# Optimization experiments

Measured on AMD Instinct MI355X. Metric: run time of the kernel, lower is better.

Reference implementation:

```python
import jax, jax.numpy as jnp
import numpy as np

B, S, D = 2, 2048, 1024
H = 16
HD = D // H  # 64
ROPE_BASE = 10000.0


def rotate_half(x):
    x1, x2 = jnp.split(x, 2, axis=-1)
    return jnp.concatenate((-x2, x1), axis=-1)


def rope_cos_sin(seq_len, dim, dtype):
    inv_freq = 1.0 / (ROPE_BASE ** (jnp.arange(0, dim, 2, dtype=jnp.float32) / dim))
    t = jnp.arange(seq_len, dtype=jnp.float32)
    freqs = jnp.einsum('i,j->ij', t, inv_freq)          # [S, dim/2]
    emb = jnp.concatenate((freqs, freqs), axis=-1)      # [S, dim]
    return jnp.cos(emb).astype(dtype), jnp.sin(emb).astype(dtype)


def setup_inputs() -> dict:
    key = jax.random.key(0)
    ks = jax.random.split(key, 5)
    std = 0.02
    return {
        'x': jax.random.normal(ks[0], (B, S, D), dtype=jnp.float32),
        'wq': jax.random.normal(ks[1], (D, D), dtype=jnp.float32) * std,
        'wk': jax.random.normal(ks[2], (D, D), dtype=jnp.float32) * std,
        'wv': jax.random.normal(ks[3], (D, D), dtype=jnp.float32) * std,
        'wo': jax.random.normal(ks[4], (D, D), dtype=jnp.float32) * std,
    }


def reference(x, wq, wk, wv, wo):
    b, s, d = x.shape
    # Q/K/V projections (nn.Linear: x @ W.T)
    q = jnp.einsum('bsd,ed->bse', x, wq).reshape(b, s, H, HD).transpose(0, 2, 1, 3)
    k = jnp.einsum('bsd,ed->bse', x, wk).reshape(b, s, H, HD).transpose(0, 2, 1, 3)
    v = jnp.einsum('bsd,ed->bse', x, wv).reshape(b, s, H, HD).transpose(0, 2, 1, 3)
    # RoPE
    cos, sin = rope_cos_sin(s, HD, x.dtype)  # [s, HD]
    cos = cos[None, None]  # [1,1,s,HD]
    sin = sin[None, None]
    q = q * cos + rotate_half(q) * sin
    k = k * cos + rotate_half(k) * sin
    # Causal SDPA
    scale = HD ** -0.5
    scores = jnp.einsum('bhqd,bhkd->bhqk', q, k) * scale
    causal = jnp.tril(jnp.ones((s, s), dtype=bool))
    scores = jnp.where(causal[None, None], scores, jnp.finfo(scores.dtype).min)
    attn = jax.nn.softmax(scores, axis=-1)
    out = jnp.einsum('bhqk,bhkd->bhqd', attn, v)
    out = out.transpose(0, 2, 1, 3).reshape(b, s, d)
    return jnp.einsum('bsd,ed->bse', out, wo)
```

## Files before the change

kernel.cpp:

```cpp
#include <hip/hip_runtime.h>
#include <hip/hip_bf16.h>
#include <cstdint>
#include <cstddef>

#define BDIM 2
#define SDIM 2048
#define DDIM 1024
#define HN   16
#define HDIM 64

using bf16 = __bf16;
typedef __attribute__((ext_vector_type(8))) __bf16 bf16x8;
typedef __attribute__((ext_vector_type(4))) __bf16 bf16x4;
typedef __attribute__((ext_vector_type(4))) float  f32x4;

#define MFMA16(a, b, c) __builtin_amdgcn_mfma_f32_16x16x32_bf16((a), (b), (c), 0, 0, 0)

#define ASYNC16(g, l)                                                          \
  __builtin_amdgcn_global_load_lds(                                            \
      (const __attribute__((address_space(1))) void*)(g),                      \
      (__attribute__((address_space(3))) void*)(l), 16, 0, 0)

#define QSCALE 0.1803368801111204f

struct Ptr5 { const float* p[5]; };
__global__ __launch_bounds__(256) void cvt_all(Ptr5 srcs, bf16* __restrict__ xb,
                                               bf16* __restrict__ wb) {
  const int NX4 = (BDIM * SDIM * DDIM) / 4;
  int i = blockIdx.x * 256 + threadIdx.x;
  const float* src;
  bf16* dst;
  int j;
  if (i < NX4) {
    src = srcs.p[0]; dst = xb; j = i;
  } else {
    int k = i - NX4;
    int seg = k >> 18;
    j = k & 262143;
    src = srcs.p[seg + 1];
    dst = wb + (size_t)seg * (DDIM * DDIM) / 1;
    dst += 0;
    j = j;
    dst = wb + (size_t)seg * (DDIM * DDIM);
  }
  float4 v = ((const float4*)src)[j];
  bf16x4 o = {(__bf16)v.x, (__bf16)v.y, (__bf16)v.z, (__bf16)v.w};
  *(bf16x4*)(dst + (size_t)j * 4) = o;
}

__global__ __launch_bounds__(256) void rope_table(float* __restrict__ cosT,
                                                  float* __restrict__ sinT) {
  int i = blockIdx.x * 256 + threadIdx.x;
  int s = i >> 5, j = i & 31;
  float inv = powf(10000.f, -(float)j * (1.f / 32.f));
  float a = (float)s * inv;
  float sn, c;
  sincosf(a, &sn, &c);
  cosT[s * 64 + j]      = c;
  cosT[s * 64 + j + 32] = c;
  sinT[s * 64 + j]      = sn;
  sinT[s * 64 + j + 32] = sn;
}

__global__ __launch_bounds__(256) void fixup_qk(bf16* __restrict__ q,
                                                bf16* __restrict__ k,
                                                const float* __restrict__ cosT,
                                                const float* __restrict__ sinT) {
  const int bh = blockIdx.y;
  const int s = blockIdx.x * 32 + (threadIdx.x >> 3);
  const int j0 = (threadIdx.x & 7) * 4;
  const size_t base = ((size_t)bh * SDIM + s) * HDIM;
  const float4 c4 = *(const float4*)(cosT + s * 64 + j0);
  const float4 s4 = *(const float4*)(sinT + s * 64 + j0);
  const float cc[4] = {c4.x, c4.y, c4.z, c4.w};
  const float ss[4] = {s4.x, s4.y, s4.z, s4.w};

  bf16x4 qlo = *(bf16x4*)(q + base + j0);
  bf16x4 qhi = *(bf16x4*)(q + base + j0 + 32);
  bf16x4 klo = *(bf16x4*)(k + base + j0);
  bf16x4 khi = *(bf16x4*)(k + base + j0 + 32);
  bf16x4 rql, rqh, rkl, rkh;
#pragma unroll
  for (int e = 0; e < 4; ++e) {
    float a = (float)qlo[e], b = (float)qhi[e];
    rql[e] = (__bf16)((a * cc[e] - b * ss[e]) * QSCALE);
    rqh[e] = (__bf16)((b * cc[e] + a * ss[e]) * QSCALE);
    a = (float)klo[e]; b = (float)khi[e];
    rkl[e] = (__bf16)(a * cc[e] - b * ss[e]);
    rkh[e] = (__bf16)(b * cc[e] + a * ss[e]);
  }
  *(bf16x4*)(q + base + j0)      = rql;
  *(bf16x4*)(q + base + j0 + 32) = rqh;
  *(bf16x4*)(k + base + j0)      = rkl;
  *(bf16x4*)(k + base + j0 + 32) = rkh;
}

__global__ __launch_bounds__(256) void gemm_qkv(const bf16* __restrict__ A,
                                                const bf16* __restrict__ B0,
                                                bf16* __restrict__ C0,
                                                bf16* __restrict__ Vt) {
  constexpr int K = 1024;
  __shared__ __align__(16) bf16 As[128 * 64];
  __shared__ __align__(16) bf16 Bs[128 * 64];
  const int tid = threadIdx.x;
  const int l = tid & 63, w = tid >> 6;
  const int wr = w >> 1, wc = w & 1;
  const int lr = l & 15, lg = l >> 4;
  const int bm = blockIdx.y * 128;
  const int bn = blockIdx.x * 128;
  const bf16* Bw = B0 + (size_t)blockIdx.z * (1024 * 1024);

  f32x4 acc[4][4] = {};

  for (int k0 = 0; k0 < K; k0 += 64) {
    __syncthreads();
#pragma unroll
    for (int i = 0; i < 4; ++i) {
      int idx = i * 2048 + tid * 8;
      int row = idx >> 6, col = idx & 63;
      ASYNC16(A + (size_t)(bm + row) * K + (k0 + col), As + idx);
      ASYNC16(Bw + (size_t)(bn + row) * K + (k0 + col), Bs + idx);
    }
    __syncthreads();
#pragma unroll
    for (int c = 0; c < 2; ++c) {
      bf16x8 af[4], bfr[4];
#pragma unroll
      for (int m = 0; m < 4; ++m)
        af[m] = *(const bf16x8*)(As + (wr * 64 + m * 16 + lr) * 64 + c * 32 + lg * 8);
#pragma unroll
      for (int n = 0; n < 4; ++n)
        bfr[n] = *(const bf16x8*)(Bs + (wc * 64 + n * 16 + lr) * 64 + c * 32 + lg * 8);
      __builtin_amdgcn_s_setprio(1);
#pragma unroll
      for (int m = 0; m < 4; ++m)
#pragma unroll
        for (int n = 0; n < 4; ++n)
          acc[m][n] = MFMA16(af[m], bfr[n], acc[m][n]);
      __builtin_amdgcn_s_setprio(0);
    }
  }

  const int z = blockIdx.z;
  if (z < 2) {
    bf16* C = C0 + (size_t)z * ((size_t)BDIM * SDIM * DDIM);
#pragma unroll
    for (int m = 0; m < 4; ++m)
#pragma unroll
      for (int n = 0; n < 4; ++n)
#pragma unroll
        for (int r = 0; r < 4; ++r) {
          int row = bm + wr * 64 + m * 16 + lg * 4 + r;
          int col = bn + wc * 64 + n * 16 + lr;
          size_t off = (((size_t)(row >> 11) * HN + (col >> 6)) * SDIM + (row & (SDIM - 1))) * HDIM + (col & 63);
          C[off] = (__bf16)acc[m][n][r];
        }
  } else {
#pragma unroll
    for (int m = 0; m < 4; ++m) {
      const int row0 = bm + wr * 64 + m * 16 + lg * 4;
      const int bb = row0 >> 11, s0 = row0 & (SDIM - 1);
#pragma unroll
      for (int n = 0; n < 4; ++n) {
        const int col = bn + wc * 64 + n * 16 + lr;
        const int h = col >> 6, hd = col & 63;
        bf16x4 pv = {(__bf16)acc[m][n][0], (__bf16)acc[m][n][1],
                     (__bf16)acc[m][n][2], (__bf16)acc[m][n][3]};
        *(bf16x4*)(Vt + ((size_t)(bb * HN + h) * HDIM + hd) * SDIM + s0) = pv;
      }
    }
  }
}

__global__ __launch_bounds__(512) void gemm_out(const bf16* __restrict__ A,
                                                const bf16* __restrict__ Bw,
                                                float* __restrict__ C) {
  constexpr int K = 1024;
  __shared__ __align__(16) bf16 As[128 * 64];
  __shared__ __align__(16) bf16 Bs[128 * 64];
  const int tid = threadIdx.x;
  const int l = tid & 63, w = tid >> 6;
  const int wr = w >> 1, wc = w & 1;
  const int lr = l & 15, lg = l >> 4;
  const int bm = blockIdx.y * 128;
  const int bn = blockIdx.x * 128;

  f32x4 acc[2][4] = {};

  for (int k0 = 0; k0 < K; k0 += 64) {
    __syncthreads();
#pragma unroll
    for (int i = 0; i < 2; ++i) {
      int idx = i * 4096 + tid * 8;
      int row = idx >> 6, col = idx & 63;
      ASYNC16(A + (size_t)(bm + row) * K + (k0 + col), As + idx);
      ASYNC16(Bw + (size_t)(bn + row) * K + (k0 + col), Bs + idx);
    }
    __syncthreads();
#pragma unroll
    for (int c = 0; c < 2; ++c) {
      bf16x8 af[2], bfr[4];
#pragma unroll
      for (int m = 0; m < 2; ++m)
        af[m] = *(const bf16x8*)(As + (wr * 32 + m * 16 + lr) * 64 + c * 32 + lg * 8);
#pragma unroll
      for (int n = 0; n < 4; ++n)
        bfr[n] = *(const bf16x8*)(Bs + (wc * 64 + n * 16 + lr) * 64 + c * 32 + lg * 8);
      __builtin_amdgcn_s_setprio(1);
#pragma unroll
      for (int m = 0; m < 2; ++m)
#pragma unroll
        for (int n = 0; n < 4; ++n)
          acc[m][n] = MFMA16(af[m], bfr[n], acc[m][n]);
      __builtin_amdgcn_s_setprio(0);
    }
  }

#pragma unroll
  for (int m = 0; m < 2; ++m)
#pragma unroll
    for (int n = 0; n < 4; ++n)
#pragma unroll
      for (int r = 0; r < 4; ++r) {
        int row = bm + wr * 32 + m * 16 + lg * 4 + r;
        int col = bn + wc * 64 + n * 16 + lr;
        C[(size_t)row * DDIM + col] = acc[m][n][r];
      }
}

__global__ __launch_bounds__(512) void attn_fwd(const bf16* __restrict__ qg,
                                                const bf16* __restrict__ kg,
                                                const bf16* __restrict__ vtg,
                                                bf16* __restrict__ og) {
  __shared__ __align__(16) bf16 Sl[2][3][4096];
  __shared__ __align__(16) bf16 Pl[8][1024];

  const int tid = threadIdx.x;
  const int l = tid & 63, w = tid >> 6;
  const int g = w >> 2, wg = w & 3;
  const int lr = l & 15, lg = l >> 4;
  const int bh = blockIdx.x;
  const int qt = 31 - blockIdx.y;
  const int q0 = qt * 64;
  const size_t hb = (size_t)bh * SDIM * HDIM;
  const bf16* Q  = qg + hb;
  const bf16* Kp = kg + hb;
  const bf16* Vp = vtg + hb;
  const int b = bh >> 4, h = bh & 15;
  bf16* Pw = &Pl[w][0];
  const int swz = lr & 7;

  const int mm0 = 2 * wg, mm1 = 2 * wg + 1;
  const int f0 = mm0 & 3, c0 = mm0 >> 2;
  const int f1 = mm1 & 3, c1 = mm1 >> 2;
  const int lo0 = mm0 * 512 + l * 8;
  const int lo1 = mm1 * 512 + l * 8;
  bf16* const SlG = &Sl[g][0][0];

  bf16x8 qf[2];
#pragma unroll
  for (int c = 0; c < 2; ++c)
    qf[c] = *(const bf16x8*)(Q + (size_t)(q0 + wg * 16 + lr) * HDIM + c * 32 + lg * 8);

  f32x4 o[4] = {};
  float m = -3e38f, lsum = 0.f;

  const int ng   = (qt >= g) ? ((qt - g) >> 1) + 1 : 0;
  const int smax = (qt >> 1) + 1;

  const bf16* kN0 = Kp + (size_t)(f0 * 16 + lr) * HDIM + c0 * 32 + lg * 8 + (size_t)g * 64 * HDIM;
  const bf16* kN1 = Kp + (size_t)(f1 * 16 + lr) * HDIM + c1 * 32 + lg * 8 + (size_t)g * 64 * HDIM;
  const bf16* vN0 = Vp + (size_t)(f0 * 16 + lr) * SDIM + c0 * 32 + lg * 8 + g * 64;
  const bf16* vN1 = Vp + (size_t)(f1 * 16 + lr) * SDIM + c1 * 32 + lg * 8 + g * 64;

  if (ng > 0) {
    ASYNC16(kN0, SlG + 0 * 4096 + lo0); kN0 += 128 * HDIM;
    ASYNC16(kN1, SlG + 0 * 4096 + lo1); kN1 += 128 * HDIM;
    ASYNC16(vN0, SlG + 1 * 4096 + lo0); vN0 += 128;
    ASYNC16(vN1, SlG + 1 * 4096 + lo1); vN1 += 128;
  }
  __syncthreads();

  int ks = 0, vs = 1;
  for (int s = 0; s < smax; ++s) {
    const int t = 2 * s + g;
    const bool act = (s < ng);
    const int kn = 3 - ks - vs;
    const bool hasNext = act && (s + 1 < ng);

    if (hasNext) {
      ASYNC16(kN0, SlG + kn * 4096 + lo0); kN0 += 128 * HDIM;
      ASYNC16(kN1, SlG + kn * 4096 + lo1); kN1 += 128 * HDIM;
    }

    const bool diag = (t == qt);
    const int fLim = diag ? wg : 3;

    f32x4 sc[4] = {};
    if (act) {
      __builtin_amdgcn_s_setprio(1);
#pragma unroll
      for (int c = 0; c < 2; ++c)
#pragma unroll
        for (int f = 0; f < 4; ++f)
          if (f <= fLim) {
            bf16x8 kfr = *(const bf16x8*)(SlG + ks * 4096 + (c * 4 + f) * 512 + l * 8);
            sc[f] = MFMA16(kfr, qf[c], sc[f]);
          }
      __builtin_amdgcn_s_setprio(0);
    }

    __builtin_amdgcn_s_barrier();
    __builtin_amdgcn_sched_barrier(0);

    if (hasNext) {
      ASYNC16(vN0, SlG + ks * 4096 + lo0); vN0 += 128;
      ASYNC16(vN1, SlG + ks * 4096 + lo1); vN1 += 128;
    }

    if (act) {
      if (diag) {
#pragma unroll
        for (int f = 0; f < 4; ++f)
#pragma unroll
          for (int r = 0; r < 4; ++r) {
            if (f > wg)
              sc[f][r] = -3e38f;
            else if (f == wg)
              sc[f][r] = (lg * 4 + r <= lr) ? sc[f][r] : -3e38f;
          }
      }

      float mxl = -3e38f;
#pragma unroll
      for (int f = 0; f < 4; ++f)
#pragma unroll
        for (int r = 0; r < 4; ++r) mxl = fmaxf(mxl, sc[f][r]);

      if (!__all(mxl - m <= 8.f)) {
        float mx = fmaxf(mxl, __shfl_xor(mxl, 16));
        mx = fmaxf(mx, __shfl_xor(mx, 32));
        float mnew = fmaxf(m, mx);
        float corr = exp2f(m - mnew);
        m = mnew;
        lsum *= corr;
        float cb[4];
#pragma unroll
        for (int r = 0; r < 4; ++r) cb[r] = __shfl(corr, lg * 4 + r);
#pragma unroll
        for (int n = 0; n < 4; ++n)
#pragma unroll
          for (int r = 0; r < 4; ++r) o[n][r] *= cb[r];
      }

      float rs = 0.f;
#pragma unroll
      for (int f = 0; f < 4; ++f) {
        float p0 = exp2f(sc[f][0] - m);
        float p1 = exp2f(sc[f][1] - m);
        float p2 = exp2f(sc[f][2] - m);
        float p3 = exp2f(sc[f][3] - m);
        rs += (p0 + p1) + (p2 + p3);
        bf16x4 pv = {(__bf16)p0, (__bf16)p1, (__bf16)p2, (__bf16)p3};
        const int ch = f * 2 + (lg >> 1);
        *(bf16x4*)(Pw + lr * 64 + ((ch ^ swz) << 3) + (lg & 1) * 4) = pv;
      }
      lsum += rs;

      const int cLim = diag ? (wg >> 1) : 1;
      __builtin_amdgcn_s_setprio(1);
#pragma unroll
      for (int c = 0; c < 2; ++c)
        if (c <= cLim) {
          bf16x8 pf = *(const bf16x8*)(Pw + lr * 64 + (((c * 4 + lg) ^ swz) << 3));
#pragma unroll
          for (int n = 0; n < 4; ++n) {
            bf16x8 vfr = *(const bf16x8*)(SlG + vs * 4096 + (c * 4 + n) * 512 + l * 8);
            o[n] = MFMA16(pf, vfr, o[n]);
          }
        }
      __builtin_amdgcn_s_setprio(0);
    }

    __syncthreads();
    vs = ks;
    ks = kn;
  }

  float* Osh = (float*)&Sl[0][0][0];
  float* Msh = Osh + 4096;
  float* Lsh = Msh + 256;

  if (g == 1) {
    Msh[wg * 64 + l] = m;
    Lsh[wg * 64 + l] = lsum;
#pragma unroll
    for (int n = 0; n < 4; ++n)
#pragma unroll
      for (int r = 0; r < 4; ++r)
        Osh[((wg * 4 + n) * 4 + r) * 64 + l] = o[n][r];
  }
  __syncthreads();

  if (g == 0) {
    float m1 = Msh[wg * 64 + l], l1 = Lsh[wg * 64 + l];
    float mt = fmaxf(m, m1);
    float a0 = exp2f(m - mt), a1 = exp2f(m1 - mt);
    float lt = lsum * a0 + l1 * a1;
    lt += __shfl_xor(lt, 16);
    lt += __shfl_xor(lt, 32);
    float a0b[4], a1b[4], ltb[4];
#pragma unroll
    for (int r = 0; r < 4; ++r) {
      a0b[r] = __shfl(a0, lg * 4 + r);
      a1b[r] = __shfl(a1, lg * 4 + r);
      ltb[r] = __shfl(lt, lg * 4 + r);
    }
#pragma unroll
    for (int r = 0; r < 4; ++r) {
      float rl = 1.f / ltb[r];
      int qr = q0 + 16 * wg + lg * 4 + r;
#pragma unroll
      for (int n = 0; n < 4; ++n) {
        float o1 = Osh[((wg * 4 + n) * 4 + r) * 64 + l];
        og[((size_t)(b * SDIM + qr)) * DDIM + h * HDIM + n * 16 + lr] =
            (__bf16)((o[n][r] * a0b[r] + o1 * a1b[r]) * rl);
      }
    }
  }
}

extern "C" void kernel_launch(void* const* d_in, const int* in_sizes, int n_in,
                              void* d_out, int out_size, void* d_ws, size_t ws_size,
                              hipStream_t stream) {
  const float* x  = (const float*)d_in[0];
  const float* wq = (const float*)d_in[1];
  const float* wk = (const float*)d_in[2];
  const float* wv = (const float*)d_in[3];
  const float* wo = (const float*)d_in[4];

  char* ws = (char*)d_ws;
  const size_t MB = 1024 * 1024;
  bf16* xb   = (bf16*)(ws + 0);
  bf16* wqb  = (bf16*)(ws + 8 * MB);
  bf16* wob  = (bf16*)(ws + 14 * MB);
  bf16* qb   = (bf16*)(ws + 16 * MB);
  bf16* kb   = (bf16*)(ws + 24 * MB);
  bf16* vtb  = (bf16*)(ws + 32 * MB);
  bf16* ob   = (bf16*)(ws + 40 * MB);
  float* cosT = (float*)(ws + 48 * MB);
  float* sinT = (float*)(ws + 49 * MB);

  const int NX = BDIM * SDIM * DDIM;
  const int NW = DDIM * DDIM;

  Ptr5 srcs{{x, wq, wk, wv, wo}};
  cvt_all<<<(NX / 4 + NW) / 256, 256, 0, stream>>>(srcs, xb, wqb);
  rope_table<<<(SDIM * 32) / 256, 256, 0, stream>>>(cosT, sinT);
  gemm_qkv<<<dim3(8, 32, 3), 256, 0, stream>>>(xb, wqb, qb, vtb);
  fixup_qk<<<dim3(SDIM / 32, 32), 256, 0, stream>>>(qb, kb, cosT, sinT);
  attn_fwd<<<dim3(32, 32), 512, 0, stream>>>(qb, kb, vtb, ob);
  gemm_out<<<dim3(8, 32), 512, 0, stream>>>(ob, wob, (float*)d_out);
}
```

Before: 131.5 us.

## Load V fragments directly to registers and stage QKV epilogue through LDS

In the attention kernel, V tiles are no longer staged through shared memory. Each wave loads its V fragments straight from global memory into registers, which removes one LDS buffer and the mid-iteration barrier. The QKV GEMM epilogue for Q and K now writes through a padded shared-memory tile so each thread issues 16-byte row stores instead of scattered 2-byte stores. Direct V loads add global-load latency to each iteration and duplicate V reads across waves in exchange for less LDS traffic and fewer barriers. A dead-code cleanup in the conversion kernel is included.

```diff
diff --git a/kernel.cpp b/kernel.cpp
--- a/kernel.cpp
+++ b/kernel.cpp
@@ -38,9 +38,6 @@
     int seg = k >> 18;
     j = k & 262143;
     src = srcs.p[seg + 1];
-    dst = wb + (size_t)seg * (DDIM * DDIM) / 1;
-    dst += 0;
-    j = j;
     dst = wb + (size_t)seg * (DDIM * DDIM);
   }
   float4 v = ((const float4*)src)[j];
@@ -100,8 +97,9 @@
                                                 bf16* __restrict__ C0,
                                                 bf16* __restrict__ Vt) {
   constexpr int K = 1024;
-  __shared__ __align__(16) bf16 As[128 * 64];
-  __shared__ __align__(16) bf16 Bs[128 * 64];
+  __shared__ __align__(16) bf16 Sh[128 * 136];
+  bf16* const As = Sh;
+  bf16* const Bs = Sh + 8192;
   const int tid = threadIdx.x;
   const int l = tid & 63, w = tid >> 6;
   const int wr = w >> 1, wc = w & 1;
@@ -143,18 +141,25 @@
 
   const int z = blockIdx.z;
   if (z < 2) {
-    bf16* C = C0 + (size_t)z * ((size_t)BDIM * SDIM * DDIM);
+    __syncthreads();
 #pragma unroll
     for (int m = 0; m < 4; ++m)
 #pragma unroll
       for (int n = 0; n < 4; ++n)
 #pragma unroll
-        for (int r = 0; r < 4; ++r) {
-          int row = bm + wr * 64 + m * 16 + lg * 4 + r;
-          int col = bn + wc * 64 + n * 16 + lr;
-          size_t off = (((size_t)(row >> 11) * HN + (col >> 6)) * SDIM + (row & (SDIM - 1))) * HDIM + (col & 63);
-          C[off] = (__bf16)acc[m][n][r];
-        }
+        for (int r = 0; r < 4; ++r)
+          Sh[(wr * 64 + m * 16 + lg * 4 + r) * 136 + wc * 64 + n * 16 + lr] =
+              (__bf16)acc[m][n][r];
+    __syncthreads();
+    const int row_l = tid >> 1, cb = (tid & 1) * 64;
+    const int row = bm + row_l;
+    const int bb = row >> 11, s = row & (SDIM - 1);
+    const int h = (bn >> 6) + (tid & 1);
+    bf16* Cb = C0 + (size_t)z * ((size_t)BDIM * SDIM * DDIM) +
+               ((size_t)(bb * HN + h) * SDIM + s) * HDIM;
+#pragma unroll
+    for (int kk = 0; kk < 8; ++kk)
+      *(bf16x8*)(Cb + kk * 8) = *(const bf16x8*)(Sh + row_l * 136 + cb + kk * 8);
   } else {
 #pragma unroll
     for (int m = 0; m < 4; ++m) {
@@ -232,7 +237,7 @@
                                                 const bf16* __restrict__ kg,
                                                 const bf16* __restrict__ vtg,
                                                 bf16* __restrict__ og) {
-  __shared__ __align__(16) bf16 Sl[2][3][4096];
+  __shared__ __align__(16) bf16 Ks[2][2][4096];
   __shared__ __align__(16) bf16 Pl[8][1024];
 
   const int tid = threadIdx.x;
@@ -255,7 +260,7 @@
   const int f1 = mm1 & 3, c1 = mm1 >> 2;
   const int lo0 = mm0 * 512 + l * 8;
   const int lo1 = mm1 * 512 + l * 8;
-  bf16* const SlG = &Sl[g][0][0];
+  bf16* const KsG = &Ks[g][0][0];
 
   bf16x8 qf[2];
 #pragma unroll
@@ -270,31 +275,36 @@
 
   const bf16* kN0 = Kp + (size_t)(f0 * 16 + lr) * HDIM + c0 * 32 + lg * 8 + (size_t)g * 64 * HDIM;
   const bf16* kN1 = Kp + (size_t)(f1 * 16 + lr) * HDIM + c1 * 32 + lg * 8 + (size_t)g * 64 * HDIM;
-  const bf16* vN0 = Vp + (size_t)(f0 * 16 + lr) * SDIM + c0 * 32 + lg * 8 + g * 64;
-  const bf16* vN1 = Vp + (size_t)(f1 * 16 + lr) * SDIM + c1 * 32 + lg * 8 + g * 64;
+  const bf16* vA[4];
+#pragma unroll
+  for (int n = 0; n < 4; ++n)
+    vA[n] = Vp + (size_t)(n * 16 + lr) * SDIM + g * 64 + lg * 8;
 
   if (ng > 0) {
-    ASYNC16(kN0, SlG + 0 * 4096 + lo0); kN0 += 128 * HDIM;
-    ASYNC16(kN1, SlG + 0 * 4096 + lo1); kN1 += 128 * HDIM;
-    ASYNC16(vN0, SlG + 1 * 4096 + lo0); vN0 += 128;
-    ASYNC16(vN1, SlG + 1 * 4096 + lo1); vN1 += 128;
+    ASYNC16(kN0, KsG + lo0); kN0 += 128 * HDIM;
+    ASYNC16(kN1, KsG + lo1); kN1 += 128 * HDIM;
   }
   __syncthreads();
 
-  int ks = 0, vs = 1;
+  int cur = 0;
   for (int s = 0; s < smax; ++s) {
     const int t = 2 * s + g;
     const bool act = (s < ng);
-    const int kn = 3 - ks - vs;
     const bool hasNext = act && (s + 1 < ng);
 
     if (hasNext) {
-      ASYNC16(kN0, SlG + kn * 4096 + lo0); kN0 += 128 * HDIM;
-      ASYNC16(kN1, SlG + kn * 4096 + lo1); kN1 += 128 * HDIM;
+      ASYNC16(kN0, KsG + (cur ^ 1) * 4096 + lo0); kN0 += 128 * HDIM;
+      ASYNC16(kN1, KsG + (cur ^ 1) * 4096 + lo1); kN1 += 128 * HDIM;
     }
 
     const bool diag = (t == qt);
     const int fLim = diag ? wg : 3;
+
+    bf16x8 v0[4], v1[4];
+    if (act) {
+#pragma unroll
+      for (int n = 0; n < 4; ++n) v0[n] = *(const bf16x8*)(vA[n]);
+    }
 
     f32x4 sc[4] = {};
     if (act) {
@@ -304,21 +314,15 @@
 #pragma unroll
         for (int f = 0; f < 4; ++f)
           if (f <= fLim) {
-            bf16x8 kfr = *(const bf16x8*)(SlG + ks * 4096 + (c * 4 + f) * 512 + l * 8);
+            bf16x8 kfr = *(const bf16x8*)(KsG + cur * 4096 + (c * 4 + f) * 512 + l * 8);
             sc[f] = MFMA16(kfr, qf[c], sc[f]);
           }
       __builtin_amdgcn_s_setprio(0);
-    }
-
-    __builtin_amdgcn_s_barrier();
-    __builtin_amdgcn_sched_barrier(0);
-
-    if (hasNext) {
-      ASYNC16(vN0, SlG + ks * 4096 + lo0); vN0 += 128;
-      ASYNC16(vN1, SlG + ks * 4096 + lo1); vN1 += 128;
-    }
-
-    if (act) {
+#pragma unroll
+      for (int n = 0; n < 4; ++n) v1[n] = *(const bf16x8*)(vA[n] + 32);
+#pragma unroll
+      for (int n = 0; n < 4; ++n) vA[n] += 128;
+
       if (diag) {
 #pragma unroll
         for (int f = 0; f < 4; ++f)
@@ -367,27 +371,25 @@
       }
       lsum += rs;
 
-      const int cLim = diag ? (wg >> 1) : 1;
       __builtin_amdgcn_s_setprio(1);
-#pragma unroll
-      for (int c = 0; c < 2; ++c)
-        if (c <= cLim) {
-          bf16x8 pf = *(const bf16x8*)(Pw + lr * 64 + (((c * 4 + lg) ^ swz) << 3));
-#pragma unroll
-          for (int n = 0; n < 4; ++n) {
-            bf16x8 vfr = *(const bf16x8*)(SlG + vs * 4096 + (c * 4 + n) * 512 + l * 8);
-            o[n] = MFMA16(pf, vfr, o[n]);
-          }
-        }
+      {
+        bf16x8 pf = *(const bf16x8*)(Pw + lr * 64 + ((lg ^ swz) << 3));
+#pragma unroll
+        for (int n = 0; n < 4; ++n) o[n] = MFMA16(pf, v0[n], o[n]);
+      }
+      if (!diag || wg >= 2) {
+        bf16x8 pf = *(const bf16x8*)(Pw + lr * 64 + (((4 + lg) ^ swz) << 3));
+#pragma unroll
+        for (int n = 0; n < 4; ++n) o[n] = MFMA16(pf, v1[n], o[n]);
+      }
       __builtin_amdgcn_s_setprio(0);
     }
 
     __syncthreads();
-    vs = ks;
-    ks = kn;
-  }
-
-  float* Osh = (float*)&Sl[0][0][0];
+    cur ^= 1;
+  }
+
+  float* Osh = (float*)&Ks[0][0][0];
   float* Msh = Osh + 4096;
   float* Lsh = Msh + 256;
 
```

After: 174.6 us. 32.8% more time.

## Fuse RoPE and Q scaling into QKV GEMM epilogue via LDS staging

Applied to the files above, without the earlier changes.

Removes the separate fixup_qk kernel by applying RoPE rotation (with the softmax scale folded into the Q table) inside the QKV GEMM epilogue. Accumulators are staged through a padded shared tile so each thread writes a full 64-wide head row with vectorized 16-byte stores, replacing the scattered 2-byte stores. The rope table becomes interleaved cos/sin float2 with a prescaled Q variant. This saves a kernel launch and a full read/write pass over Q and K, at the cost of larger LDS usage and an extra sync in the epilogue.

```diff
diff --git a/kernel.cpp b/kernel.cpp
--- a/kernel.cpp
+++ b/kernel.cpp
@@ -38,9 +38,6 @@
     int seg = k >> 18;
     j = k & 262143;
     src = srcs.p[seg + 1];
-    dst = wb + (size_t)seg * (DDIM * DDIM) / 1;
-    dst += 0;
-    j = j;
     dst = wb + (size_t)seg * (DDIM * DDIM);
   }
   float4 v = ((const float4*)src)[j];
@@ -48,60 +45,28 @@
   *(bf16x4*)(dst + (size_t)j * 4) = o;
 }
 
-__global__ __launch_bounds__(256) void rope_table(float* __restrict__ cosT,
-                                                  float* __restrict__ sinT) {
+__global__ __launch_bounds__(256) void rope_table(float2* __restrict__ cq,
+                                                  float2* __restrict__ ck) {
   int i = blockIdx.x * 256 + threadIdx.x;
   int s = i >> 5, j = i & 31;
   float inv = powf(10000.f, -(float)j * (1.f / 32.f));
   float a = (float)s * inv;
   float sn, c;
   sincosf(a, &sn, &c);
-  cosT[s * 64 + j]      = c;
-  cosT[s * 64 + j + 32] = c;
-  sinT[s * 64 + j]      = sn;
-  sinT[s * 64 + j + 32] = sn;
-}
-
-__global__ __launch_bounds__(256) void fixup_qk(bf16* __restrict__ q,
-                                                bf16* __restrict__ k,
-                                                const float* __restrict__ cosT,
-                                                const float* __restrict__ sinT) {
-  const int bh = blockIdx.y;
-  const int s = blockIdx.x * 32 + (threadIdx.x >> 3);
-  const int j0 = (threadIdx.x & 7) * 4;
-  const size_t base = ((size_t)bh * SDIM + s) * HDIM;
-  const float4 c4 = *(const float4*)(cosT + s * 64 + j0);
-  const float4 s4 = *(const float4*)(sinT + s * 64 + j0);
-  const float cc[4] = {c4.x, c4.y, c4.z, c4.w};
-  const float ss[4] = {s4.x, s4.y, s4.z, s4.w};
-
-  bf16x4 qlo = *(bf16x4*)(q + base + j0);
-  bf16x4 qhi = *(bf16x4*)(q + base + j0 + 32);
-  bf16x4 klo = *(bf16x4*)(k + base + j0);
-  bf16x4 khi = *(bf16x4*)(k + base + j0 + 32);
-  bf16x4 rql, rqh, rkl, rkh;
-#pragma unroll
-  for (int e = 0; e < 4; ++e) {
-    float a = (float)qlo[e], b = (float)qhi[e];
-    rql[e] = (__bf16)((a * cc[e] - b * ss[e]) * QSCALE);
-    rqh[e] = (__bf16)((b * cc[e] + a * ss[e]) * QSCALE);
-    a = (float)klo[e]; b = (float)khi[e];
-    rkl[e] = (__bf16)(a * cc[e] - b * ss[e]);
-    rkh[e] = (__bf16)(b * cc[e] + a * ss[e]);
-  }
-  *(bf16x4*)(q + base + j0)      = rql;
-  *(bf16x4*)(q + base + j0 + 32) = rqh;
-  *(bf16x4*)(k + base + j0)      = rkl;
-  *(bf16x4*)(k + base + j0 + 32) = rkh;
+  ck[i] = make_float2(c, sn);
+  cq[i] = make_float2(c * QSCALE, sn * QSCALE);
 }
 
 __global__ __launch_bounds__(256) void gemm_qkv(const bf16* __restrict__ A,
                                                 const bf16* __restrict__ B0,
                                                 bf16* __restrict__ C0,
-                                                bf16* __restrict__ Vt) {
+                                                bf16* __restrict__ Vt,
+                                                const float2* __restrict__ cqT,
+                                                const float2* __restrict__ ckT) {
   constexpr int K = 1024;
-  __shared__ __align__(16) bf16 As[128 * 64];
-  __shared__ __align__(16) bf16 Bs[128 * 64];
+  __shared__ __align__(16) bf16 Sh[128 * 136];
+  bf16* const As = Sh;
+  bf16* const Bs = Sh + 8192;
   const int tid = threadIdx.x;
   const int l = tid & 63, w = tid >> 6;
   const int wr = w >> 1, wc = w & 1;
@@ -143,18 +108,40 @@
 
   const int z = blockIdx.z;
   if (z < 2) {
-    bf16* C = C0 + (size_t)z * ((size_t)BDIM * SDIM * DDIM);
+    __syncthreads();
 #pragma unroll
     for (int m = 0; m < 4; ++m)
 #pragma unroll
       for (int n = 0; n < 4; ++n)
 #pragma unroll
-        for (int r = 0; r < 4; ++r) {
-          int row = bm + wr * 64 + m * 16 + lg * 4 + r;
-          int col = bn + wc * 64 + n * 16 + lr;
-          size_t off = (((size_t)(row >> 11) * HN + (col >> 6)) * SDIM + (row & (SDIM - 1))) * HDIM + (col & 63);
-          C[off] = (__bf16)acc[m][n][r];
-        }
+        for (int r = 0; r < 4; ++r)
+          Sh[(wr * 64 + m * 16 + lg * 4 + r) * 136 + wc * 64 + n * 16 + lr] =
+              (__bf16)acc[m][n][r];
+    __syncthreads();
+    const int row_l = tid >> 1, half = tid & 1;
+    const int row = bm + row_l;
+    const int bb = row >> 11, s = row & (SDIM - 1);
+    const int h = (bn >> 6) + half;
+    const float2* T = z ? ckT : cqT;
+    bf16x8 v[8];
+#pragma unroll
+    for (int kk = 0; kk < 8; ++kk)
+      v[kk] = *(const bf16x8*)(Sh + row_l * 136 + half * 64 + kk * 8);
+    bf16x8 ov[8];
+#pragma unroll
+    for (int kk = 0; kk < 4; ++kk)
+#pragma unroll
+      for (int e = 0; e < 8; ++e) {
+        float2 cs = T[s * 32 + kk * 8 + e];
+        float lo = (float)v[kk][e], hi = (float)v[kk + 4][e];
+        ov[kk][e]     = (__bf16)(lo * cs.x - hi * cs.y);
+        ov[kk + 4][e] = (__bf16)(hi * cs.x + lo * cs.y);
+      }
+    bf16* Cb = C0 + (size_t)z * ((size_t)BDIM * SDIM * DDIM) +
+               ((size_t)(bb * HN + h) * SDIM + s) * HDIM;
+#pragma unroll
+    for (int kk = 0; kk < 8; ++kk)
+      *(bf16x8*)(Cb + kk * 8) = ov[kk];
   } else {
 #pragma unroll
     for (int m = 0; m < 4; ++m) {
@@ -448,17 +435,16 @@
   bf16* kb   = (bf16*)(ws + 24 * MB);
   bf16* vtb  = (bf16*)(ws + 32 * MB);
   bf16* ob   = (bf16*)(ws + 40 * MB);
-  float* cosT = (float*)(ws + 48 * MB);
-  float* sinT = (float*)(ws + 49 * MB);
+  float2* cqT = (float2*)(ws + 48 * MB);
+  float2* ckT = (float2*)(ws + 48 * MB + 512 * 1024);
 
   const int NX = BDIM * SDIM * DDIM;
   const int NW = DDIM * DDIM;
 
   Ptr5 srcs{{x, wq, wk, wv, wo}};
   cvt_all<<<(NX / 4 + NW) / 256, 256, 0, stream>>>(srcs, xb, wqb);
-  rope_table<<<(SDIM * 32) / 256, 256, 0, stream>>>(cosT, sinT);
-  gemm_qkv<<<dim3(8, 32, 3), 256, 0, stream>>>(xb, wqb, qb, vtb);
-  fixup_qk<<<dim3(SDIM / 32, 32), 256, 0, stream>>>(qb, kb, cosT, sinT);
+  rope_table<<<(SDIM * 32) / 256, 256, 0, stream>>>(cqT, ckT);
+  gemm_qkv<<<dim3(8, 32, 3), 256, 0, stream>>>(xb, wqb, qb, vtb, cqT, ckT);
   attn_fwd<<<dim3(32, 32), 512, 0, stream>>>(qb, kb, vtb, ob);
   gemm_out<<<dim3(8, 32), 512, 0, stream>>>(ob, wob, (float*)d_out);
 }
```

Measured after the change: 129.1 us. No clear change (-1.8%).
